# Performance work log

Hardware: AMD Instinct MI355X
Metric: run time of the kernel (lower is better)

Reference implementation:

```python
import jax, jax.numpy as jnp
import numpy as np
import math

HEADS = 8


def rope(t):
    # t: [..., seq, dim]; lucidrains-style interleaved rotary embedding
    seq, dim = t.shape[-2], t.shape[-1]
    inv = 1.0 / (10000.0 ** (jnp.arange(0, dim, 2, dtype=jnp.float32) / dim))
    freqs = jnp.arange(seq, dtype=jnp.float32)[:, None] * inv[None, :]  # [seq, dim/2]
    freqs = jnp.repeat(freqs, 2, axis=-1)                               # [seq, dim]
    cos, sin = jnp.cos(freqs), jnp.sin(freqs)
    t2 = t.reshape(t.shape[:-1] + (dim // 2, 2))
    rot = jnp.stack([-t2[..., 1], t2[..., 0]], axis=-1).reshape(t.shape)
    return t * cos + rot * sin


def conv1x3(x, w):
    # x: [b,c,h,w], w: [out_c,in_c,1,3], padding (0,1), no bias
    return jax.lax.conv_general_dilated(
        x, w, window_strides=(1, 1), padding=((0, 0), (1, 1)),
        dimension_numbers=('NCHW', 'OIHW', 'NCHW'))


def mcl_pw(x, w_pw):
    # per-channel linear on feature axis h: w_pw [c, out_f, in_f]
    return jnp.einsum('bchw,cgh->bcgw', x, w_pw)


def setup_inputs() -> dict:
    key = jax.random.key(0)
    ks = jax.random.split(key, 10)
    b, c, f, w = 2, 8, 256, 1024
    s = 0.05
    return {
        'x': jax.random.normal(ks[0], (b, c, f, w), dtype=jnp.float32),
        'q_pw': jax.random.normal(ks[1], (c, f, f), dtype=jnp.float32) * s,
        'q_cw': jax.random.normal(ks[2], (c, c, 1, 3), dtype=jnp.float32) * s,
        'k_pw': jax.random.normal(ks[3], (c, f, f), dtype=jnp.float32) * s,
        'k_cw': jax.random.normal(ks[4], (c, c, 1, 3), dtype=jnp.float32) * s,
        'v_pw': jax.random.normal(ks[5], (c, f, f), dtype=jnp.float32) * s,
        'v_cw': jax.random.normal(ks[6], (c, c, 1, 3), dtype=jnp.float32) * s,
        'out_pw': jax.random.normal(ks[7], (c, f, f), dtype=jnp.float32) * s,
        'out_dw': jax.random.normal(ks[8], (c, c), dtype=jnp.float32) * s,
    }


def reference(x, q_pw, q_cw, k_pw, k_cw, v_pw, v_cw, out_pw, out_dw):
    b, c, h, w = x.shape
    hd = h // HEADS

    def split_heads(y):  # [b,c,h,w] -> [b,c,heads,w,hd]
        return y.transpose(0, 1, 3, 2).reshape(b, c, w, HEADS, hd).transpose(0, 1, 3, 2, 4)

    q = rope(split_heads(conv1x3(mcl_pw(x, q_pw), q_cw)))
    k = rope(split_heads(conv1x3(mcl_pw(x, k_pw), k_cw)))
    v = split_heads(conv1x3(mcl_pw(x, v_pw), v_cw))

    # non-standard scaling by sqrt(h) = sqrt(features)
    qk = jnp.einsum('bcnqd,bcnkd->bcnqk', q, k) / math.sqrt(h)
    a = jnp.einsum('bcnqk,bcnkd->bcnqd', jax.nn.softmax(qk, axis=-1), v)
    a = a.transpose(0, 1, 3, 2, 4).reshape(b, c, w, h).transpose(0, 1, 3, 2)  # [b,c,h,w]

    # out_proj: depthwise channel mix then per-channel positionwise linear
    out = jnp.einsum('bchw,dc->bdhw', a, out_dw)
    out = mcl_pw(out, out_pw)
    return out
```

## Files before the change

kernel.cpp:

```cpp
#include <hip/hip_runtime.h>
#include <hip/hip_bf16.h>

#define B 2
#define C 8
#define F 256
#define W 1024
#define NH 8
#define HD 32

typedef float f32x4 __attribute__((ext_vector_type(4)));
typedef short sh8 __attribute__((ext_vector_type(8)));
typedef short sh4 __attribute__((ext_vector_type(4)));
typedef unsigned short u16;

#define QSCALE 0.09016843880556021f

static __device__ __forceinline__ float fexp2(float x) {
#if __has_builtin(__builtin_amdgcn_exp2f)
  return __builtin_amdgcn_exp2f(x);
#else
  return __expf(x * 0.69314718056f);
#endif
}

static __device__ __forceinline__ u16 f2b(float x) {
  union { __hip_bfloat16 h; u16 u; } v;
  v.h = __float2bfloat16(x);
  return v.u;
}
static __device__ __forceinline__ sh4 pack4(float p0, float p1, float p2, float p3) {
  union { __hip_bfloat162 h2[2]; sh4 s; } u;
  u.h2[0] = __float22bfloat162_rn(make_float2(p0, p1));
  u.h2[1] = __float22bfloat162_rn(make_float2(p2, p3));
  return u.s;
}
static __device__ __forceinline__ float b2f(u16 x) {
  union { unsigned int u; float f; } v;
  v.u = ((unsigned int)x) << 16;
  return v.f;
}
static __device__ __forceinline__ float ubits(unsigned int u) {
  union { unsigned int u; float f; } v;
  v.u = u;
  return v.f;
}

static __device__ __forceinline__ f32x4 mfma32(sh8 a, sh8 b, f32x4 c) {
  return __builtin_amdgcn_mfma_f32_16x16x32_bf16(a, b, c, 0, 0, 0);
}

static __device__ __forceinline__ f32x4 mfma16(sh4 a, sh4 b, f32x4 c) {
#if __has_builtin(__builtin_amdgcn_mfma_f32_16x16x16bf16_1k)
  return __builtin_amdgcn_mfma_f32_16x16x16bf16_1k(a, b, c, 0, 0, 0);
#else
  f32x4 d;
  asm("v_mfma_f32_16x16x16_bf16 %0, %1, %2, %3" : "=v"(d) : "v"(a), "v"(b), "v"(c));
  return d;
#endif
}

static __device__ __forceinline__ void gload16(const u16* g, u16* l, int ln) {
#if __has_builtin(__builtin_amdgcn_global_load_lds)
  __builtin_amdgcn_global_load_lds((const __attribute__((address_space(1))) void*)g,
                                   (__attribute__((address_space(3))) void*)l, 16, 0, 0);
#else
  *(sh8*)(l + ln * 8) = *(const sh8*)g;
#endif
}

__global__ __launch_bounds__(256) void prep(const float* __restrict__ x, u16* __restrict__ xt,
                                            const float* __restrict__ s0, const float* __restrict__ s1,
                                            const float* __restrict__ s2, const float* __restrict__ s3,
                                            u16* __restrict__ d0, u16* __restrict__ d1,
                                            u16* __restrict__ d2, u16* __restrict__ d3,
                                            float2* __restrict__ TAB) {
  const int bid = blockIdx.x;
  const int t = threadIdx.x;
  if (bid < 4096) {
    const int bc = bid >> 8, rem = bid & 255;
    const int h0 = ((rem >> 5) & 7) * 32, w0 = (rem & 31) * 32;
    __shared__ u16 sm[32][34];
    const int a = t & 31, bql = t >> 5;
    const float* src = x + ((size_t)bc * F + h0) * W + w0;
#pragma unroll
    for (int p = 0; p < 4; ++p) {
      const int hl = bql + p * 8;
      sm[a][hl] = f2b(src[(size_t)hl * W + a]);
    }
    __syncthreads();
    u16* dst = xt + ((size_t)bc * W + w0) * F + h0;
#pragma unroll
    for (int p = 0; p < 4; ++p) {
      const int wl = bql + p * 8;
      dst[(size_t)wl * F + a] = sm[wl][a];
    }
  } else if (bid < 6144) {
    const int i = bid - 4096;
    const int which = i >> 9;
    const float* s = which == 0 ? s0 : which == 1 ? s1 : which == 2 ? s2 : s3;
    u16* d = which == 0 ? d0 : which == 1 ? d1 : which == 2 ? d2 : d3;
    const int idx = (i & 511) * 256 + t;
    const float4 v = reinterpret_cast<const float4*>(s)[idx];
    union { u16 h[4]; uint2 u; } o;
    o.h[0] = f2b(v.x); o.h[1] = f2b(v.y); o.h[2] = f2b(v.z); o.h[3] = f2b(v.w);
    reinterpret_cast<uint2*>(d)[idx] = o.u;
  } else {
    const int idx = (bid - 6144) * 256 + t;
    const int j = idx >> 10, w = idx & 1023;
    const float inv = powf(10000.f, -(float)(2 * j) / 32.f);
    float sn, cs;
    sincosf((float)w * inv, &sn, &cs);
    TAB[idx] = make_float2(cs, sn);
  }
}

template <bool OUTBF>
__global__ __launch_bounds__(256) void gemm_bt(const u16* __restrict__ Aw,
                                               const u16* __restrict__ Bt,
                                               void* __restrict__ Cc) {
  const int bc = blockIdx.z;
  const int proj = blockIdx.y >> 1;
  const int g0 = (blockIdx.y & 1) * 128;
  const int w0 = blockIdx.x * 64;
  const int t = threadIdx.x;
  const int ln = t & 63, wid = t >> 6;
  const int lr = ln & 15, lk = (ln >> 4) * 8;
  const int wr = wid >> 1, wc = wid & 1;

  const u16* Ab = Aw + (size_t)proj * C * F * F + (size_t)(bc & 7) * F * F;
  const u16* Bb = Bt + (size_t)bc * W * F;

  __shared__ u16 sA[16 * 512];
  __shared__ u16 sB[8 * 512];

  const u16* ga0 = Ab + (size_t)(g0 + (wid * 2 + 0) * 16 + lr) * F + lk;
  const u16* ga1 = Ab + (size_t)(g0 + (wid * 2 + 1) * 16 + lr) * F + lk;
  const u16* gb0 = Bb + (size_t)(w0 + wid * 16 + lr) * F + lk;

  f32x4 acc[4][2] = {};

  for (int h0 = 0; h0 < F; h0 += 64) {
    __syncthreads();
    gload16(ga0 + h0,      &sA[(0 * 8 + wid * 2 + 0) * 512], ln);
    gload16(ga0 + h0 + 32, &sA[(1 * 8 + wid * 2 + 0) * 512], ln);
    gload16(ga1 + h0,      &sA[(0 * 8 + wid * 2 + 1) * 512], ln);
    gload16(ga1 + h0 + 32, &sA[(1 * 8 + wid * 2 + 1) * 512], ln);
    gload16(gb0 + h0,      &sB[(0 * 4 + wid) * 512], ln);
    gload16(gb0 + h0 + 32, &sB[(1 * 4 + wid) * 512], ln);
    __syncthreads();
#pragma unroll
    for (int kh = 0; kh < 2; ++kh) {
      sh8 af[4], bfr[2];
#pragma unroll
      for (int mi = 0; mi < 4; ++mi)
        af[mi] = *(const sh8*)&sA[((kh * 8 + wr * 4 + mi) * 64 + ln) * 8];
#pragma unroll
      for (int ni = 0; ni < 2; ++ni)
        bfr[ni] = *(const sh8*)&sB[((kh * 4 + wc * 2 + ni) * 64 + ln) * 8];
#pragma unroll
      for (int mi = 0; mi < 4; ++mi)
#pragma unroll
        for (int ni = 0; ni < 2; ++ni)
          acc[mi][ni] = mfma32(af[mi], bfr[ni], acc[mi][ni]);
    }
  }

  const int lq = ln >> 4;
  const size_t cbase = ((size_t)proj * B * C + bc) * F * W;
  if (OUTBF) {
    u16* Cb = (u16*)Cc + cbase;
#pragma unroll
    for (int mi = 0; mi < 4; ++mi)
#pragma unroll
      for (int ni = 0; ni < 2; ++ni)
#pragma unroll
        for (int r = 0; r < 4; ++r)
          Cb[(size_t)(g0 + wr * 64 + mi * 16 + lq * 4 + r) * W + w0 + wc * 32 + ni * 16 + lr] =
              f2b(acc[mi][ni][r]);
  } else {
    float* Cb = (float*)Cc + cbase;
#pragma unroll
    for (int mi = 0; mi < 4; ++mi)
#pragma unroll
      for (int ni = 0; ni < 2; ++ni)
#pragma unroll
        for (int r = 0; r < 4; ++r)
          Cb[(size_t)(g0 + wr * 64 + mi * 16 + lq * 4 + r) * W + w0 + wc * 32 + ni * 16 + lr] =
              acc[mi][ni][r];
  }
}

__global__ __launch_bounds__(256) void conv2(const u16* __restrict__ IN,
                                             const float* __restrict__ CWq,
                                             const float* __restrict__ CWk,
                                             const float* __restrict__ CWv,
                                             const float* __restrict__ TAB,
                                             u16* __restrict__ OUT) {
  const int f2 = blockIdx.x;
  const int z = blockIdx.y;
  const int proj = z >> 1, b = z & 1;
  const float* CW = proj == 0 ? CWq : proj == 1 ? CWk : CWv;
  const size_t NB = (size_t)B * C * F * W;
  const u16* INp = IN + (size_t)proj * NB;
  u16* OUTp = OUT + (size_t)proj * NB;
  const int do_rope = (proj < 2);
  const float scale = (proj == 0) ? QSCALE : 1.0f;
  const int f0 = f2 * 2;
  const int t = threadIdx.x;

  __shared__ u16 s[2][C][1040];
  __shared__ float cw[C][C][3];
  if (t < C * C * 3) ((float*)cw)[t] = CW[t];
  if (t < 16) {
    const int fi = t >> 3, c2 = t & 7;
    s[fi][c2][7] = 0;
    s[fi][c2][1032] = 0;
  }
  {
    const int l = t & 127, rsel = t >> 7;
#pragma unroll
    for (int p = 0; p < 8; ++p) {
      const int row = p * 2 + rsel;
      const int fi = row >> 3, c2 = row & 7;
      const u16* src = INp + ((size_t)(b * C + c2) * F + f0 + fi) * W + l * 8;
      *(sh8*)&s[fi][c2][8 + l * 8] = *(const sh8*)src;
    }
  }
  __syncthreads();

  float acc[2][C][4] = {};
#pragma unroll
  for (int c = 0; c < C; ++c) {
    float v[2][6];
#pragma unroll
    for (int fi = 0; fi < 2; ++fi) {
      const unsigned int* r32 = (const unsigned int*)&s[fi][c][0];
      const unsigned int r0 = r32[2 * t + 3];
      const unsigned int r1 = r32[2 * t + 4];
      const unsigned int r2 = r32[2 * t + 5];
      const unsigned int r3 = r32[2 * t + 6];
      v[fi][0] = ubits(r0 & 0xffff0000u);
      v[fi][1] = ubits(r1 << 16);
      v[fi][2] = ubits(r1 & 0xffff0000u);
      v[fi][3] = ubits(r2 << 16);
      v[fi][4] = ubits(r2 & 0xffff0000u);
      v[fi][5] = ubits(r3 << 16);
    }
#pragma unroll
    for (int d = 0; d < C; ++d) {
      const float c0 = cw[d][c][0], c1 = cw[d][c][1], c2_ = cw[d][c][2];
#pragma unroll
      for (int fi = 0; fi < 2; ++fi)
#pragma unroll
        for (int o = 0; o < 4; ++o)
          acc[fi][d][o] += v[fi][o] * c0 + v[fi][o + 1] * c1 + v[fi][o + 2] * c2_;
    }
  }

  float cs[4] = {1.f, 1.f, 1.f, 1.f}, sn[4] = {0.f, 0.f, 0.f, 0.f};
  if (do_rope) {
    const int j = f2 & 15;
    const float4* tp = (const float4*)(TAB + (size_t)(j * 1024 + 4 * t) * 2);
    const float4 A0 = tp[0], A1 = tp[1];
    cs[0] = A0.x; sn[0] = A0.y; cs[1] = A0.z; sn[1] = A0.w;
    cs[2] = A1.x; sn[2] = A1.y; cs[3] = A1.z; sn[3] = A1.w;
  }

#pragma unroll
  for (int d = 0; d < C; ++d) {
    sh4 pk0, pk1;
#pragma unroll
    for (int o = 0; o < 4; ++o) {
      const float a0 = acc[0][d][o], a1 = acc[1][d][o];
      float o0 = a0, o1 = a1;
      if (do_rope) { o0 = a0 * cs[o] - a1 * sn[o]; o1 = a1 * cs[o] + a0 * sn[o]; }
      pk0[o] = (short)f2b(o0 * scale);
      pk1[o] = (short)f2b(o1 * scale);
    }
    u16* dst = OUTp + ((size_t)(b * C + d) * F + f0) * W + 4 * t;
    *(sh4*)dst = pk0;
    *(sh4*)(dst + W) = pk1;
  }
}

__global__ __launch_bounds__(512) void attn_bf(const u16* __restrict__ Q,
                                               const u16* __restrict__ K,
                                               const u16* __restrict__ Vv,
                                               float* __restrict__ O) {
  const int bc = blockIdx.z, n = blockIdx.y, q0 = blockIdx.x * 128;
  const int t = threadIdx.x, ln = t & 63, wid = t >> 6;
  const int lc = ln & 15, g4 = (ln >> 4) * 4;
  const int dq = (ln >> 4) * 8;
  const size_t base = ((size_t)bc * F + n * HD) * W;

  __shared__ u16 Kl[2][64 * 40];
  __shared__ u16 Vl[2][32 * 76];

  const int skey = t & 63, dq4 = (t >> 6) * 4;
  const u16* gK = K + base + (size_t)dq4 * W + skey;
  const int sd = t >> 4, kc4 = (t & 15) * 4;
  const u16* gV = Vv + base + (size_t)sd * W + kc4;

  const int qw = q0 + wid * 16 + lc;
  sh8 qf;
#pragma unroll
  for (int j = 0; j < 8; ++j) qf[j] = (short)Q[base + (size_t)(dq + j) * W + qw];

  const sh4 ones = {0x3F80, 0x3F80, 0x3F80, 0x3F80};
  f32x4 o0 = {0.f, 0.f, 0.f, 0.f}, o1 = {0.f, 0.f, 0.f, 0.f};
  f32x4 dn = {0.f, 0.f, 0.f, 0.f};

  {
    sh4 hv;
#pragma unroll
    for (int j = 0; j < 4; ++j) hv[j] = (short)gK[(size_t)j * W];
    *(sh4*)&Kl[0][skey * 40 + dq4] = hv;
    *(sh4*)&Vl[0][sd * 76 + kc4] = *(const sh4*)gV;
  }
  __syncthreads();

  for (int tile = 0; tile < 16; ++tile) {
    const int cur = tile & 1;
    sh4 hvK, hvV;
    if (tile < 15) {
      const int off = (tile + 1) * 64;
#pragma unroll
      for (int j = 0; j < 4; ++j) hvK[j] = (short)gK[(size_t)j * W + off];
      hvV = *(const sh4*)(gV + off);
    }

    f32x4 sf[4];
    __builtin_amdgcn_s_setprio(1);
#pragma unroll
    for (int kh = 0; kh < 4; ++kh) {
      const sh8 kf = *(const sh8*)&Kl[cur][(kh * 16 + lc) * 40 + dq];
      f32x4 z = {0.f, 0.f, 0.f, 0.f};
      sf[kh] = mfma32(kf, qf, z);
    }
    __builtin_amdgcn_s_setprio(0);

    sh4 pb[4];
#pragma unroll
    for (int kh = 0; kh < 4; ++kh) {
      const float p0 = fexp2(sf[kh][0]);
      const float p1 = fexp2(sf[kh][1]);
      const float p2 = fexp2(sf[kh][2]);
      const float p3 = fexp2(sf[kh][3]);
      pb[kh] = pack4(p0, p1, p2, p3);
    }

    __builtin_amdgcn_s_setprio(1);
#pragma unroll
    for (int kh = 0; kh < 4; ++kh) {
      const sh4 vf0 = *(const sh4*)&Vl[cur][lc * 76 + kh * 16 + g4];
      const sh4 vf1 = *(const sh4*)&Vl[cur][(16 + lc) * 76 + kh * 16 + g4];
      o0 = mfma16(pb[kh], vf0, o0);
      o1 = mfma16(pb[kh], vf1, o1);
      dn = mfma16(pb[kh], ones, dn);
    }
    __builtin_amdgcn_s_setprio(0);

    if (tile < 15) {
      *(sh4*)&Kl[cur ^ 1][skey * 40 + dq4] = hvK;
      *(sh4*)&Vl[cur ^ 1][sd * 76 + kc4] = hvV;
    }
    __syncthreads();
  }

#pragma unroll
  for (int r = 0; r < 4; ++r) {
    const float inv = 1.f / dn[r];
    const int qrow = q0 + wid * 16 + g4 + r;
    O[base + (size_t)lc * W + qrow] = o0[r] * inv;
    O[base + (size_t)(16 + lc) * W + qrow] = o1[r] * inv;
  }
}

__global__ __launch_bounds__(256) void chanmix_t(const float* __restrict__ A,
                                                 const float* __restrict__ DW,
                                                 u16* __restrict__ O1) {
  const int b = blockIdx.z, f0 = blockIdx.y * 32, w0 = blockIdx.x * 32;
  const int t = threadIdx.x;
  __shared__ u16 sm[C][32][34];
  float dwv[C][C];
#pragma unroll
  for (int d = 0; d < C; ++d)
#pragma unroll
    for (int c = 0; c < C; ++c) dwv[d][c] = DW[d * C + c];

  const int wl = t & 31, fs = t >> 5;
#pragma unroll
  for (int p = 0; p < 4; ++p) {
    const int fl = p * 8 + fs;
    float av[C];
#pragma unroll
    for (int c = 0; c < C; ++c)
      av[c] = A[((size_t)(b * C + c) * F + f0 + fl) * W + w0 + wl];
#pragma unroll
    for (int d = 0; d < C; ++d) {
      float s = 0.f;
#pragma unroll
      for (int c = 0; c < C; ++c) s += av[c] * dwv[d][c];
      sm[d][wl][fl] = f2b(s);
    }
  }
  __syncthreads();
  const int fl2 = t & 31, ws = t >> 5;
#pragma unroll
  for (int d = 0; d < C; ++d)
#pragma unroll
    for (int p = 0; p < 4; ++p) {
      const int wl2 = p * 8 + ws;
      O1[((size_t)(b * C + d) * W + w0 + wl2) * F + f0 + fl2] = sm[d][wl2][fl2];
    }
}

extern "C" void kernel_launch(void* const* d_in, const int* in_sizes, int n_in,
                              void* d_out, int out_size, void* d_ws, size_t ws_size,
                              hipStream_t stream) {
  const float* x      = (const float*)d_in[0];
  const float* q_pw   = (const float*)d_in[1];
  const float* q_cw   = (const float*)d_in[2];
  const float* k_pw   = (const float*)d_in[3];
  const float* k_cw   = (const float*)d_in[4];
  const float* v_pw   = (const float*)d_in[5];
  const float* v_cw   = (const float*)d_in[6];
  const float* out_pw = (const float*)d_in[7];
  const float* out_dw = (const float*)d_in[8];

  const size_t NB = (size_t)B * C * F * W;
  const size_t CFF = (size_t)C * F * F;

  u16* xt   = (u16*)d_ws;
  u16* wqkv = xt + NB;
  u16* wo   = wqkv + 3 * CFF;
  u16* t0b  = wo + CFF;
  u16* qkvb = t0b + 3 * NB;
  float* tab = (float*)(qkvb + 3 * NB);
  float* obuf = (float*)t0b;
  u16* o1t  = xt;

  prep<<<4096 + 2048 + 64, 256, 0, stream>>>(
      x, xt, q_pw, k_pw, v_pw, out_pw, wqkv, wqkv + CFF, wqkv + 2 * CFF, wo, (float2*)tab);

  gemm_bt<true><<<dim3(W / 64, 6, B * C), 256, 0, stream>>>(wqkv, xt, t0b);
  conv2<<<dim3(F / 2, 3 * B), 256, 0, stream>>>(t0b, q_cw, k_cw, v_cw, tab, qkvb);

  attn_bf<<<dim3(W / 128, NH, B * C), 512, 0, stream>>>(qkvb, qkvb + NB, qkvb + 2 * NB, obuf);

  chanmix_t<<<dim3(W / 32, F / 32, B), 256, 0, stream>>>(obuf, out_dw, o1t);
  gemm_bt<false><<<dim3(W / 64, 2, B * C), 256, 0, stream>>>(wo, o1t, d_out);
}
```

Before: 106.6 us.

## Write attention output transposed and drop LDS transpose in channel mix

The attention kernel now stores its fp32 output in [bc, w, f] order instead of [bc, f, w]. This lets the channel-mix kernel read float4 rows directly and write bf16 in the transposed layout without a shared-memory transpose or barrier. The cost moves into attention's epilogue: each lane now writes scattered 4-byte values with a stride of F, giving poorer coalescing there. The channel-mix kernel becomes a simpler, vectorized streaming pass. The change relies on pack4 already existing in the hidden code.

After: 104.9 us. No clear change (-1.6%).

```diff
diff --git a/kernel.cpp b/kernel.cpp
--- a/kernel.cpp
+++ b/kernel.cpp
@@ -286,7 +286,7 @@
 __global__ __launch_bounds__(512) void attn_bf(const u16* __restrict__ Q,
                                                const u16* __restrict__ K,
                                                const u16* __restrict__ Vv,
-                                               float* __restrict__ O) {
+                                               float* __restrict__ OT) {
   const int bc = blockIdx.z, n = blockIdx.y, q0 = blockIdx.x * 128;
   const int t = threadIdx.x, ln = t & 63, wid = t >> 6;
   const int lc = ln & 15, g4 = (ln >> 4) * 4;
@@ -367,52 +367,44 @@
     __syncthreads();
   }
 
+  const size_t obase = (size_t)bc * W * F + n * HD;
 #pragma unroll
   for (int r = 0; r < 4; ++r) {
     const float inv = 1.f / dn[r];
     const int qrow = q0 + wid * 16 + g4 + r;
-    O[base + (size_t)lc * W + qrow] = o0[r] * inv;
-    O[base + (size_t)(16 + lc) * W + qrow] = o1[r] * inv;
-  }
-}
-
-__global__ __launch_bounds__(256) void chanmix_t(const float* __restrict__ A,
-                                                 const float* __restrict__ DW,
-                                                 u16* __restrict__ O1) {
-  const int b = blockIdx.z, f0 = blockIdx.y * 32, w0 = blockIdx.x * 32;
-  const int t = threadIdx.x;
-  __shared__ u16 sm[C][32][34];
+    OT[obase + (size_t)qrow * F + lc] = o0[r] * inv;
+    OT[obase + (size_t)qrow * F + 16 + lc] = o1[r] * inv;
+  }
+}
+
+__global__ __launch_bounds__(256) void chanmix2(const float* __restrict__ A,
+                                                const float* __restrict__ DW,
+                                                u16* __restrict__ O1) {
+  const int b = blockIdx.y;
+  const int w = blockIdx.x * 4 + (threadIdx.x >> 6);
+  const int f4 = (threadIdx.x & 63) * 4;
   float dwv[C][C];
 #pragma unroll
   for (int d = 0; d < C; ++d)
 #pragma unroll
     for (int c = 0; c < C; ++c) dwv[d][c] = DW[d * C + c];
 
-  const int wl = t & 31, fs = t >> 5;
-#pragma unroll
-  for (int p = 0; p < 4; ++p) {
-    const int fl = p * 8 + fs;
-    float av[C];
-#pragma unroll
-    for (int c = 0; c < C; ++c)
-      av[c] = A[((size_t)(b * C + c) * F + f0 + fl) * W + w0 + wl];
-#pragma unroll
-    for (int d = 0; d < C; ++d) {
-      float s = 0.f;
-#pragma unroll
-      for (int c = 0; c < C; ++c) s += av[c] * dwv[d][c];
-      sm[d][wl][fl] = f2b(s);
-    }
-  }
-  __syncthreads();
-  const int fl2 = t & 31, ws = t >> 5;
-#pragma unroll
-  for (int d = 0; d < C; ++d)
-#pragma unroll
-    for (int p = 0; p < 4; ++p) {
-      const int wl2 = p * 8 + ws;
-      O1[((size_t)(b * C + d) * W + w0 + wl2) * F + f0 + fl2] = sm[d][wl2][fl2];
-    }
+  float4 av[C];
+#pragma unroll
+  for (int c = 0; c < C; ++c)
+    av[c] = *(const float4*)&A[(((size_t)(b * C + c)) * W + w) * F + f4];
+#pragma unroll
+  for (int d = 0; d < C; ++d) {
+    float sx = 0.f, sy = 0.f, sz = 0.f, sw = 0.f;
+#pragma unroll
+    for (int c = 0; c < C; ++c) {
+      sx += av[c].x * dwv[d][c];
+      sy += av[c].y * dwv[d][c];
+      sz += av[c].z * dwv[d][c];
+      sw += av[c].w * dwv[d][c];
+    }
+    *(sh4*)&O1[(((size_t)(b * C + d)) * W + w) * F + f4] = pack4(sx, sy, sz, sw);
+  }
 }
 
 extern "C" void kernel_launch(void* const* d_in, const int* in_sizes, int n_in,
@@ -448,6 +440,6 @@
 
   attn_bf<<<dim3(W / 128, NH, B * C), 512, 0, stream>>>(qkvb, qkvb + NB, qkvb + 2 * NB, obuf);
 
-  chanmix_t<<<dim3(W / 32, F / 32, B), 256, 0, stream>>>(obuf, out_dw, o1t);
+  chanmix2<<<dim3(W / 4, B), 256, 0, stream>>>(obuf, out_dw, o1t);
   gemm_bt<false><<<dim3(W / 64, 2, B * C), 256, 0, stream>>>(wo, o1t, d_out);
 }
```
